# Optimization experiments

Measured on AMD Instinct MI355X. Metric: run time of the kernel, lower is better.

The kernel has to match this reference:

```python
import jax, jax.numpy as jnp
import numpy as np

B, T, E = 4, 2048, 1024
H, HS = 16, 64
FF = 4 * E
EPS = 1e-5


def _layer_norm(x, g, b):
    mu = jnp.mean(x, axis=-1, keepdims=True)
    var = jnp.mean(jnp.square(x - mu), axis=-1, keepdims=True)
    return (x - mu) * jax.lax.rsqrt(var + EPS) * g + b


def setup_inputs() -> dict:
    key = jax.random.key(0)
    ks = jax.random.split(key, 8)
    s_e = 1.0 / np.sqrt(E)
    s_hs = 1.0 / np.sqrt(H * HS)
    s_ff = 1.0 / np.sqrt(FF)
    return {
        "x": jax.random.normal(ks[0], (B, T, E), dtype=jnp.float32),
        # weights stored as [in, out] (transpose of torch's [out, in])
        "qkv_w": jax.random.uniform(ks[1], (E, 3 * H * HS), minval=-s_e, maxval=s_e),
        "attn_proj_w": jax.random.uniform(ks[2], (H * HS, E), minval=-s_hs, maxval=s_hs),
        "attn_proj_b": jax.random.uniform(ks[3], (E,), minval=-s_hs, maxval=s_hs),
        "ln1_g": jnp.ones((E,), jnp.float32),
        "ln1_b": jnp.zeros((E,), jnp.float32),
        "ln2_g": jnp.ones((E,), jnp.float32),
        "ln2_b": jnp.zeros((E,), jnp.float32),
        "ff_w1": jax.random.uniform(ks[4], (E, FF), minval=-s_e, maxval=s_e),
        "ff_b1": jax.random.uniform(ks[5], (FF,), minval=-s_e, maxval=s_e),
        "ff_w2": jax.random.uniform(ks[6], (FF, E), minval=-s_ff, maxval=s_ff),
        "ff_b2": jax.random.uniform(ks[7], (E,), minval=-s_ff, maxval=s_ff),
    }


def reference(x, qkv_w, attn_proj_w, attn_proj_b, ln1_g, ln1_b, ln2_g, ln2_b,
              ff_w1, ff_b1, ff_w2, ff_b2):
    b, t, _ = x.shape
    # --- pre-LN causal self-attention ---
    h = _layer_norm(x, ln1_g, ln1_b)
    qkv = h @ qkv_w                                  # [B,T,3*H*HS]
    q, k, v = jnp.split(qkv, 3, axis=-1)
    q = q.reshape(b, t, H, HS).transpose(0, 2, 1, 3)  # [B,H,T,HS]
    k = k.reshape(b, t, H, HS).transpose(0, 2, 1, 3)
    v = v.reshape(b, t, H, HS).transpose(0, 2, 1, 3)
    scores = jnp.einsum('bhqd,bhkd->bhqk', q, k) * (HS ** -0.5)
    causal = jnp.tril(jnp.ones((t, t), dtype=bool))
    scores = jnp.where(causal, scores, -jnp.inf)
    attn = jax.nn.softmax(scores, axis=-1)
    out = jnp.einsum('bhqk,bhkd->bhqd', attn, v)      # [B,H,T,HS]
    out = out.transpose(0, 2, 1, 3).reshape(b, t, H * HS)
    x = x + out @ attn_proj_w + attn_proj_b
    # --- pre-LN feed-forward ---
    h2 = _layer_norm(x, ln2_g, ln2_b)
    ff = jax.nn.relu(h2 @ ff_w1 + ff_b1) @ ff_w2 + ff_b2
    return x + ff
```

## Files before the change

kernel.cpp:

```cpp
#include <hip/hip_runtime.h>
#include <math.h>

#define B_ 4
#define T_ 2048
#define E_ 1024
#define H_ 16
#define HS_ 64
#define FF_ 4096
#define M_ (B_ * T_)
#define QKV3_ (3 * H_ * HS_)

typedef short bf16x8 __attribute__((ext_vector_type(8)));
typedef short bf16x4 __attribute__((ext_vector_type(4)));
typedef float f32x4 __attribute__((ext_vector_type(4)));

__device__ __forceinline__ unsigned short f2bf(float f) {
    unsigned int u = __float_as_uint(f);
    return (unsigned short)((u + 0x7fffu + ((u >> 16) & 1u)) >> 16);
}

__device__ __forceinline__ void gload16(const void* g, void* l) {
    __builtin_amdgcn_global_load_lds(
        (const __attribute__((address_space(1))) void*)g,
        (__attribute__((address_space(3))) void*)l, 16, 0, 0);
}

__global__ __launch_bounds__(256) void wT_bf16(const float* __restrict__ W,
                                               unsigned short* __restrict__ WT,
                                               int K, int N) {
    __shared__ float t[32][33];
    const int n0 = blockIdx.x * 32, k0 = blockIdx.y * 32;
    const int tid = threadIdx.x;
#pragma unroll
    for (int i = 0; i < 4; i++) {
        const int idx = i * 256 + tid;
        const int r = idx >> 5, c = idx & 31;
        t[r][c] = W[(size_t)(k0 + r) * N + n0 + c];
    }
    __syncthreads();
#pragma unroll
    for (int i = 0; i < 4; i++) {
        const int idx = i * 256 + tid;
        const int n = idx >> 5, k = idx & 31;
        WT[(size_t)(n0 + n) * K + k0 + k] = f2bf(t[k][n]);
    }
}

__global__ __launch_bounds__(256) void ln_bf16(const float* __restrict__ x,
                                               const float* __restrict__ g,
                                               const float* __restrict__ b,
                                               unsigned short* __restrict__ out) {
    const int row = blockIdx.x;
    const int tid = threadIdx.x;
    const float4 v = ((const float4*)(x + (size_t)row * E_))[tid];
    float s = v.x + v.y + v.z + v.w;
    float ss = v.x * v.x + v.y * v.y + v.z * v.z + v.w * v.w;
    for (int off = 32; off > 0; off >>= 1) {
        s += __shfl_down(s, off);
        ss += __shfl_down(ss, off);
    }
    __shared__ float rs[4], rss[4];
    const int wid = tid >> 6;
    if ((tid & 63) == 0) { rs[wid] = s; rss[wid] = ss; }
    __syncthreads();
    const float tot = rs[0] + rs[1] + rs[2] + rs[3];
    const float tot2 = rss[0] + rss[1] + rss[2] + rss[3];
    const float mean = tot * (1.0f / E_);
    const float var = tot2 * (1.0f / E_) - mean * mean;
    const float rstd = rsqrtf(var + 1e-5f);
    const float4 gv = ((const float4*)g)[tid];
    const float4 bv = ((const float4*)b)[tid];
    ushort4 o;
    o.x = f2bf((v.x - mean) * rstd * gv.x + bv.x);
    o.y = f2bf((v.y - mean) * rstd * gv.y + bv.y);
    o.z = f2bf((v.z - mean) * rstd * gv.z + bv.z);
    o.w = f2bf((v.w - mean) * rstd * gv.w + bv.w);
    ((ushort4*)(out + (size_t)row * E_))[tid] = o;
}

template <bool BIASF, bool RELU, bool RES, bool OUTBF16>
__global__ __launch_bounds__(256) void gemm_bf16(
    const unsigned short* __restrict__ A,
    const unsigned short* __restrict__ BT,
    const float* __restrict__ bias,
    const float* __restrict__ res,
    float* __restrict__ Cf,
    unsigned short* __restrict__ Cb,
    int M, int N, int K) {
    __shared__ unsigned short Al[128 * 64];
    __shared__ unsigned short Bl[128 * 64];

    const int tid = threadIdx.x;
    const int lane = tid & 63;
    const int w = tid >> 6;
    const int wm = w >> 1, wn = w & 1;

    const int gx = gridDim.x;
    const int nwg = gx * gridDim.y;
    const int lin = blockIdx.y * gx + blockIdx.x;
    const int cpx = nwg >> 3;
    const int swz = (lin & 7) * cpx + (lin >> 3);
    const int rowBase = (swz / gx) * 128, colBase = (swz % gx) * 128;

    f32x4 acc[4][4];
#pragma unroll
    for (int mt = 0; mt < 4; mt++)
#pragma unroll
        for (int nt = 0; nt < 4; nt++)
#pragma unroll
            for (int r = 0; r < 4; r++) acc[mt][nt][r] = 0.0f;

    const size_t rA = (size_t)rowBase * K;
    const size_t rB = (size_t)colBase * K;
    const int lm = lane & 15;
    const int kg = lane >> 4;

    for (int k0 = 0; k0 < K; k0 += 64) {
#pragma unroll
        for (int i = 0; i < 4; i++) {
            const int c = (w * 4 + i) * 64 + lane;
            const int r = c >> 3, s = c & 7;
            const int ss = s ^ (r & 7);
            gload16(A + rA + (size_t)r * K + k0 + ss * 8, (char*)Al + c * 16);
            gload16(BT + rB + (size_t)r * K + k0 + ss * 8, (char*)Bl + c * 16);
        }
        __syncthreads();

#pragma unroll
        for (int ks = 0; ks < 2; ks++) {
            bf16x8 af[4], bfr[4];
#pragma unroll
            for (int mt = 0; mt < 4; mt++)
                af[mt] = *(const bf16x8*)(Al + (wm * 64 + mt * 16 + lm) * 64 +
                                          (((ks * 4 + kg) ^ (lm & 7)) * 8));
#pragma unroll
            for (int nt = 0; nt < 4; nt++)
                bfr[nt] = *(const bf16x8*)(Bl + (wn * 64 + nt * 16 + lm) * 64 +
                                           (((ks * 4 + kg) ^ (lm & 7)) * 8));
#pragma unroll
            for (int mt = 0; mt < 4; mt++)
#pragma unroll
                for (int nt = 0; nt < 4; nt++)
                    acc[mt][nt] = __builtin_amdgcn_mfma_f32_16x16x32_bf16(
                        af[mt], bfr[nt], acc[mt][nt], 0, 0, 0);
        }
        __syncthreads();
    }

#pragma unroll
    for (int mt = 0; mt < 4; mt++) {
#pragma unroll
        for (int nt = 0; nt < 4; nt++) {
            const int cg = colBase + wn * 64 + nt * 16 + lm;
#pragma unroll
            for (int r = 0; r < 4; r++) {
                const int rg = rowBase + wm * 64 + mt * 16 + kg * 4 + r;
                float v = acc[mt][nt][r];
                if (BIASF) v += bias[cg];
                if (RELU) v = fmaxf(v, 0.0f);
                if (RES) v += res[(size_t)rg * N + cg];
                if (OUTBF16) Cb[(size_t)rg * N + cg] = f2bf(v);
                else Cf[(size_t)rg * N + cg] = v;
            }
        }
    }
}

__global__ __launch_bounds__(256) void attn_mfma2(const unsigned short* __restrict__ qkv,
                                                  unsigned short* __restrict__ out) {
    __shared__ unsigned short Ks[64 * 64];
    __shared__ unsigned short Vt[64 * 72];

    const int tid = threadIdx.x;
    const int lane = tid & 63;
    const int w = tid >> 6;
    const int lm = lane & 15;
    const int kg = lane >> 4;
    const int qt = 15 - blockIdx.x;
    const int bh = blockIdx.y;
    const int b = bh >> 4, h = bh & 15;
    const int bT = b * T_;
    const int q0w = qt * 128 + w * 32;
    const float K1 = 0.18033688011f;

    bf16x8 qf[2][2];
#pragma unroll
    for (int qg = 0; qg < 2; qg++) {
        const size_t qo = (size_t)(bT + q0w + qg * 16 + lm) * QKV3_ + h * HS_;
#pragma unroll
        for (int dc = 0; dc < 2; dc++)
            qf[qg][dc] = *(const bf16x8*)(qkv + qo + dc * 32 + kg * 8);
    }

    f32x4 o[2][4];
#pragma unroll
    for (int qg = 0; qg < 2; qg++)
#pragma unroll
        for (int dt = 0; dt < 4; dt++)
#pragma unroll
            for (int r = 0; r < 4; r++) o[qg][dt][r] = 0.0f;
    float m2[2] = {-INFINITY, -INFINITY};
    float l[2] = {0.0f, 0.0f};

    const int rK = tid >> 3, chK = tid & 7;
    const int sK = (chK ^ (rK & 7)) * 8;
    const int rp = tid >> 3, chV = tid & 7;
    const int vws = (2 * rp) ^ (chV << 2);

    const size_t hK = E_ + h * HS_;
    const size_t hV = 2 * E_ + h * HS_;
    bf16x8 kA, kB, vA, vB;

#define LOADT(kvb)                                                                          \
    do {                                                                                    \
        kA = *(const bf16x8*)(qkv + (size_t)(bT + (kvb) + rK) * QKV3_ + hK + chK * 8);      \
        kB = *(const bf16x8*)(qkv + (size_t)(bT + (kvb) + rK + 32) * QKV3_ + hK + chK * 8); \
        vA = *(const bf16x8*)(qkv + (size_t)(bT + (kvb) + 2 * rp) * QKV3_ + hV + chV * 8);  \
        vB = *(const bf16x8*)(qkv + (size_t)(bT + (kvb) + 2 * rp + 1) * QKV3_ + hV + chV * 8); \
    } while (0)

    const int nt = 2 * (qt + 1);
    LOADT(0);
    for (int t = 0; t < nt; t++) {
        const int kvbase = t * 64;
        __syncthreads();
        *(bf16x8*)(Ks + rK * 64 + sK) = kA;
        *(bf16x8*)(Ks + (rK + 32) * 64 + sK) = kB;
#pragma unroll
        for (int i = 0; i < 8; i++) {
            const unsigned int pv = (unsigned int)(unsigned short)vA[i] |
                                    ((unsigned int)(unsigned short)vB[i] << 16);
            *(unsigned int*)(Vt + (chV * 8 + i) * 72 + vws) = pv;
        }
        if (t + 1 < nt) LOADT((t + 1) * 64);
        __syncthreads();
        if (kvbase > q0w + 31) continue;

        bf16x8 af[4][2];
#pragma unroll
        for (int g = 0; g < 4; g++)
#pragma unroll
            for (int dc = 0; dc < 2; dc++)
                af[g][dc] = *(const bf16x8*)(Ks + (g * 16 + lm) * 64 +
                                             (((dc * 4 + kg) ^ (lm & 7)) * 8));

        bf16x8 pa[2][2];
#pragma unroll
        for (int qg = 0; qg < 2; qg++) {
            f32x4 z = {0.0f, 0.0f, 0.0f, 0.0f};
            f32x4 s[4];
#pragma unroll
            for (int g = 0; g < 4; g++) {
                s[g] = __builtin_amdgcn_mfma_f32_16x16x32_bf16(af[g][0], qf[qg][0], z, 0, 0, 0);
                s[g] = __builtin_amdgcn_mfma_f32_16x16x32_bf16(af[g][1], qf[qg][1], s[g], 0, 0, 0);
            }
            const int qrow = q0w + qg * 16 + lm;
            float sv[16];
#pragma unroll
            for (int g = 0; g < 4; g++)
#pragma unroll
                for (int r = 0; r < 4; r++) sv[g * 4 + r] = s[g][r];
            if (kvbase + 63 > q0w + qg * 16) {
#pragma unroll
                for (int g = 0; g < 4; g++)
#pragma unroll
                    for (int r = 0; r < 4; r++) {
                        const int kv = kvbase + g * 16 + kg * 4 + r;
                        if (kv > qrow) sv[g * 4 + r] = -INFINITY;
                    }
            }
            float mx = sv[0];
#pragma unroll
            for (int j = 1; j < 16; j++) mx = fmaxf(mx, sv[j]);
            mx = fmaxf(mx, __shfl_xor(mx, 16));
            mx = fmaxf(mx, __shfl_xor(mx, 32));
            const float mx2 = mx * K1;
            if (!__all(m2[qg] > -1e30f && mx2 <= m2[qg] + 11.5f)) {
                const float m2new = fmaxf(m2[qg], mx2);
                const float alpha = exp2f(m2[qg] - m2new);
#pragma unroll
                for (int r = 0; r < 4; r++) {
                    const float ar = __shfl(alpha, kg * 4 + r);
#pragma unroll
                    for (int dt = 0; dt < 4; dt++) o[qg][dt][r] *= ar;
                }
                l[qg] *= alpha;
                m2[qg] = m2new;
            }
            float p[16], ls = 0.0f;
#pragma unroll
            for (int j = 0; j < 16; j++) {
                p[j] = exp2f(fmaf(sv[j], K1, -m2[qg]));
                ls += p[j];
            }
            ls += __shfl_xor(ls, 16);
            ls += __shfl_xor(ls, 32);
            l[qg] += ls;
#pragma unroll
            for (int j = 0; j < 8; j++) {
                ((unsigned short*)&pa[qg][0])[j] = f2bf(p[j]);
                ((unsigned short*)&pa[qg][1])[j] = f2bf(p[8 + j]);
            }
        }

#pragma unroll
        for (int dt = 0; dt < 4; dt++) {
            const int drow = dt * 16 + lm;
            const unsigned short* vrow = Vt + drow * 72;
            const int xo = (kg * 4) ^ (((drow >> 3) & 7) << 2);
#pragma unroll
            for (int c = 0; c < 2; c++) {
                const bf16x4 lo = *(const bf16x4*)(vrow + c * 32 + xo);
                const bf16x4 hi = *(const bf16x4*)(vrow + c * 32 + (xo ^ 16));
                const bf16x8 vf = __builtin_shufflevector(lo, hi, 0, 1, 2, 3, 4, 5, 6, 7);
                o[0][dt] = __builtin_amdgcn_mfma_f32_16x16x32_bf16(pa[0][c], vf, o[0][dt], 0, 0, 0);
                o[1][dt] = __builtin_amdgcn_mfma_f32_16x16x32_bf16(pa[1][c], vf, o[1][dt], 0, 0, 0);
            }
        }
    }
#undef LOADT

#pragma unroll
    for (int qg = 0; qg < 2; qg++)
#pragma unroll
        for (int r = 0; r < 4; r++) {
            const float li = 1.0f / __shfl(l[qg], kg * 4 + r);
            const size_t ro = (size_t)(bT + q0w + qg * 16 + kg * 4 + r) * E_ + h * HS_;
#pragma unroll
            for (int dt = 0; dt < 4; dt++)
                out[ro + dt * 16 + lm] = f2bf(o[qg][dt][r] * li);
        }
}

extern "C" void kernel_launch(void* const* d_in, const int* in_sizes, int n_in,
                              void* d_out, int out_size, void* d_ws, size_t ws_size,
                              hipStream_t stream) {
    const float* x           = (const float*)d_in[0];
    const float* qkv_w       = (const float*)d_in[1];
    const float* attn_proj_w = (const float*)d_in[2];
    const float* attn_proj_b = (const float*)d_in[3];
    const float* ln1_g       = (const float*)d_in[4];
    const float* ln1_b       = (const float*)d_in[5];
    const float* ln2_g       = (const float*)d_in[6];
    const float* ln2_b       = (const float*)d_in[7];
    const float* ff_w1       = (const float*)d_in[8];
    const float* ff_b1       = (const float*)d_in[9];
    const float* ff_w2       = (const float*)d_in[10];
    const float* ff_b2       = (const float*)d_in[11];
    float* out = (float*)d_out;
    char* wsb = (char*)d_ws;

    unsigned short* wqkvT  = (unsigned short*)(wsb + 0);
    unsigned short* wprojT = (unsigned short*)(wsb + 6291456);
    unsigned short* wff1T  = (unsigned short*)(wsb + 8388608);
    unsigned short* wff2T  = (unsigned short*)(wsb + 16777216);
    unsigned short* hbuf   = (unsigned short*)(wsb + 25165824);
    unsigned short* attnb  = (unsigned short*)(wsb + 41943040);
    unsigned short* qkvb   = (unsigned short*)(wsb + 58720256);
    unsigned short* ff1b   = qkvb;

    wT_bf16<<<dim3(QKV3_ / 32, E_ / 32), 256, 0, stream>>>(qkv_w, wqkvT, E_, QKV3_);
    wT_bf16<<<dim3(E_ / 32, E_ / 32), 256, 0, stream>>>(attn_proj_w, wprojT, E_, E_);
    wT_bf16<<<dim3(FF_ / 32, E_ / 32), 256, 0, stream>>>(ff_w1, wff1T, E_, FF_);
    wT_bf16<<<dim3(E_ / 32, FF_ / 32), 256, 0, stream>>>(ff_w2, wff2T, FF_, E_);

    ln_bf16<<<M_, 256, 0, stream>>>(x, ln1_g, ln1_b, hbuf);
    gemm_bf16<false, false, false, true><<<dim3(QKV3_ / 128, M_ / 128), 256, 0, stream>>>(
        hbuf, wqkvT, nullptr, nullptr, nullptr, qkvb, M_, QKV3_, E_);
    attn_mfma2<<<dim3(T_ / 128, B_ * H_), 256, 0, stream>>>(qkvb, attnb);
    gemm_bf16<true, false, true, false><<<dim3(E_ / 128, M_ / 128), 256, 0, stream>>>(
        attnb, wprojT, attn_proj_b, x, out, nullptr, M_, E_, E_);
    ln_bf16<<<M_, 256, 0, stream>>>(out, ln2_g, ln2_b, hbuf);
    gemm_bf16<true, true, false, true><<<dim3(FF_ / 128, M_ / 128), 256, 0, stream>>>(
        hbuf, wff1T, ff_b1, nullptr, nullptr, ff1b, M_, FF_, E_);
    gemm_bf16<true, false, true, false><<<dim3(E_ / 128, M_ / 128), 256, 0, stream>>>(
        ff1b, wff2T, ff_b2, out, out, nullptr, M_, E_, FF_);
    (void)ws_size; (void)in_sizes; (void)n_in; (void)out_size;
}
```

Baseline: 586.8 us.

## Triple-buffer GEMM with 128x256 tiles, 512 threads; double-buffer attention K/V

The GEMM now uses 512-thread blocks with 128x256 tiles and a three-stage LDS ring. Global-to-LDS loads run two k-steps ahead, with explicit vmcnt waits, raw barriers and setprio around the MFMA blocks, to hide memory latency behind compute. The attention kernel double-buffers its K/V LDS tiles, so one barrier per iteration replaces two, and it rewrites the max and sum reductions as trees for more ILP. The GEMM LDS footprint grows to about 144KB, which limits occupancy to one block per CU, and the hand-written wait counts are fragile.

```diff
diff --git a/kernel.cpp b/kernel.cpp
--- a/kernel.cpp
+++ b/kernel.cpp
@@ -78,8 +78,16 @@
     ((ushort4*)(out + (size_t)row * E_))[tid] = o;
 }
 
+__device__ __forceinline__ void stage_half(const unsigned short* __restrict__ G,
+                                           size_t rbase, int K, int k0,
+                                           unsigned short* lds, int c) {
+    const int r = c >> 3, s = c & 7;
+    gload16(G + rbase + (size_t)r * K + k0 + ((s ^ (r & 7)) * 8),
+            (char*)lds + c * 16);
+}
+
 template <bool BIASF, bool RELU, bool RES, bool OUTBF16>
-__global__ __launch_bounds__(256) void gemm_bf16(
+__global__ __launch_bounds__(512) void gemm_v3(
     const unsigned short* __restrict__ A,
     const unsigned short* __restrict__ BT,
     const float* __restrict__ bias,
@@ -87,64 +95,98 @@
     float* __restrict__ Cf,
     unsigned short* __restrict__ Cb,
     int M, int N, int K) {
-    __shared__ unsigned short Al[128 * 64];
-    __shared__ unsigned short Bl[128 * 64];
+    __shared__ unsigned short As[3][128 * 64];
+    __shared__ unsigned short Bs[3][256 * 64];
 
     const int tid = threadIdx.x;
     const int lane = tid & 63;
     const int w = tid >> 6;
-    const int wm = w >> 1, wn = w & 1;
+    const int wm = w >> 2, wn = w & 3;
+    const int lm = lane & 15;
+    const int kg = lane >> 4;
 
     const int gx = gridDim.x;
     const int nwg = gx * gridDim.y;
     const int lin = blockIdx.y * gx + blockIdx.x;
     const int cpx = nwg >> 3;
     const int swz = (lin & 7) * cpx + (lin >> 3);
-    const int rowBase = (swz / gx) * 128, colBase = (swz % gx) * 128;
-
-    f32x4 acc[4][4];
-#pragma unroll
-    for (int mt = 0; mt < 4; mt++)
-#pragma unroll
-        for (int nt = 0; nt < 4; nt++)
-#pragma unroll
-            for (int r = 0; r < 4; r++) acc[mt][nt][r] = 0.0f;
+    const int rowBase = (swz / gx) * 128, colBase = (swz % gx) * 256;
 
     const size_t rA = (size_t)rowBase * K;
     const size_t rB = (size_t)colBase * K;
-    const int lm = lane & 15;
-    const int kg = lane >> 4;
-
-    for (int k0 = 0; k0 < K; k0 += 64) {
-#pragma unroll
-        for (int i = 0; i < 4; i++) {
-            const int c = (w * 4 + i) * 64 + lane;
-            const int r = c >> 3, s = c & 7;
-            const int ss = s ^ (r & 7);
-            gload16(A + rA + (size_t)r * K + k0 + ss * 8, (char*)Al + c * 16);
-            gload16(BT + rB + (size_t)r * K + k0 + ss * 8, (char*)Bl + c * 16);
-        }
-        __syncthreads();
-
-#pragma unroll
-        for (int ks = 0; ks < 2; ks++) {
+
+    f32x4 acc[4][4];
+#pragma unroll
+    for (int mt = 0; mt < 4; mt++)
+#pragma unroll
+        for (int nt = 0; nt < 4; nt++)
+#pragma unroll
+            for (int r = 0; r < 4; r++) acc[mt][nt][r] = 0.0f;
+
+    const int nk = K >> 6;
+#pragma unroll
+    for (int h = 0; h < 2; h++) {
+        stage_half(A, rA, K, 0, As[0], h * 512 + tid);
+        stage_half(BT, rB, K, 0, Bs[0], h * 1024 + tid);
+        stage_half(BT, rB, K, 0, Bs[0], h * 1024 + 512 + tid);
+    }
+#pragma unroll
+    for (int h = 0; h < 2; h++) {
+        stage_half(A, rA, K, 64, As[1], h * 512 + tid);
+        stage_half(BT, rB, K, 64, Bs[1], h * 1024 + tid);
+        stage_half(BT, rB, K, 64, Bs[1], h * 1024 + 512 + tid);
+    }
+    asm volatile("s_waitcnt vmcnt(6)" ::: "memory");
+    __builtin_amdgcn_s_barrier();
+    __builtin_amdgcn_sched_barrier(0);
+
+    for (int t = 0; t < nk; ++t) {
+        const int cur = t % 3;
+        const int nx2 = (t + 2) % 3;
+        const bool doStage = (t + 2 < nk);
+#pragma unroll
+        for (int ks = 0; ks < 2; ++ks) {
             bf16x8 af[4], bfr[4];
 #pragma unroll
-            for (int mt = 0; mt < 4; mt++)
-                af[mt] = *(const bf16x8*)(Al + (wm * 64 + mt * 16 + lm) * 64 +
-                                          (((ks * 4 + kg) ^ (lm & 7)) * 8));
-#pragma unroll
-            for (int nt = 0; nt < 4; nt++)
-                bfr[nt] = *(const bf16x8*)(Bl + (wn * 64 + nt * 16 + lm) * 64 +
-                                           (((ks * 4 + kg) ^ (lm & 7)) * 8));
+            for (int mt = 0; mt < 4; mt++) {
+                const int r = wm * 64 + mt * 16 + lm;
+                af[mt] = *(const bf16x8*)(As[cur] + r * 64 +
+                                          (((ks * 4 + kg) ^ (r & 7)) * 8));
+            }
+#pragma unroll
+            for (int nt = 0; nt < 4; nt++) {
+                const int r = wn * 64 + nt * 16 + lm;
+                bfr[nt] = *(const bf16x8*)(Bs[cur] + r * 64 +
+                                           (((ks * 4 + kg) ^ (r & 7)) * 8));
+            }
+            if (doStage) {
+                stage_half(A, rA, K, (t + 2) * 64, As[nx2], ks * 512 + tid);
+                stage_half(BT, rB, K, (t + 2) * 64, Bs[nx2], ks * 1024 + tid);
+                stage_half(BT, rB, K, (t + 2) * 64, Bs[nx2], ks * 1024 + 512 + tid);
+            }
+            __builtin_amdgcn_s_barrier();
+            __builtin_amdgcn_sched_barrier(0);
+            __builtin_amdgcn_s_setprio(1);
 #pragma unroll
             for (int mt = 0; mt < 4; mt++)
 #pragma unroll
                 for (int nt = 0; nt < 4; nt++)
                     acc[mt][nt] = __builtin_amdgcn_mfma_f32_16x16x32_bf16(
                         af[mt], bfr[nt], acc[mt][nt], 0, 0, 0);
-        }
-        __syncthreads();
+            __builtin_amdgcn_s_setprio(0);
+            if (ks == 0) {
+                __builtin_amdgcn_s_barrier();
+                __builtin_amdgcn_sched_barrier(0);
+            }
+        }
+        if (t + 2 < nk) {
+            asm volatile("s_waitcnt vmcnt(6)" ::: "memory");
+        } else if (t + 1 < nk) {
+            asm volatile("s_waitcnt vmcnt(0)" ::: "memory");
+        }
+        __builtin_amdgcn_sched_barrier(0);
+        __builtin_amdgcn_s_barrier();
+        __builtin_amdgcn_sched_barrier(0);
     }
 
 #pragma unroll
@@ -166,10 +208,10 @@
     }
 }
 
-__global__ __launch_bounds__(256) void attn_mfma2(const unsigned short* __restrict__ qkv,
+__global__ __launch_bounds__(256) void attn_mfma3(const unsigned short* __restrict__ qkv,
                                                   unsigned short* __restrict__ out) {
-    __shared__ unsigned short Ks[64 * 64];
-    __shared__ unsigned short Vt[64 * 72];
+    __shared__ unsigned short Ks[2][64 * 64];
+    __shared__ unsigned short Vt[2][64 * 72];
 
     const int tid = threadIdx.x;
     const int lane = tid & 63;
@@ -223,17 +265,19 @@
     LOADT(0);
     for (int t = 0; t < nt; t++) {
         const int kvbase = t * 64;
-        __syncthreads();
-        *(bf16x8*)(Ks + rK * 64 + sK) = kA;
-        *(bf16x8*)(Ks + (rK + 32) * 64 + sK) = kB;
+        const int cb = t & 1;
+        *(bf16x8*)(Ks[cb] + rK * 64 + sK) = kA;
+        *(bf16x8*)(Ks[cb] + (rK + 32) * 64 + sK) = kB;
 #pragma unroll
         for (int i = 0; i < 8; i++) {
             const unsigned int pv = (unsigned int)(unsigned short)vA[i] |
                                     ((unsigned int)(unsigned short)vB[i] << 16);
-            *(unsigned int*)(Vt + (chV * 8 + i) * 72 + vws) = pv;
+            *(unsigned int*)(Vt[cb] + (chV * 8 + i) * 72 + vws) = pv;
         }
         if (t + 1 < nt) LOADT((t + 1) * 64);
-        __syncthreads();
+        asm volatile("s_waitcnt lgkmcnt(0)" ::: "memory");
+        __builtin_amdgcn_s_barrier();
+        __builtin_amdgcn_sched_barrier(0);
         if (kvbase > q0w + 31) continue;
 
         bf16x8 af[4][2];
@@ -241,7 +285,7 @@
         for (int g = 0; g < 4; g++)
 #pragma unroll
             for (int dc = 0; dc < 2; dc++)
-                af[g][dc] = *(const bf16x8*)(Ks + (g * 16 + lm) * 64 +
+                af[g][dc] = *(const bf16x8*)(Ks[cb] + (g * 16 + lm) * 64 +
                                              (((dc * 4 + kg) ^ (lm & 7)) * 8));
 
         bf16x8 pa[2][2];
@@ -269,12 +313,14 @@
                         if (kv > qrow) sv[g * 4 + r] = -INFINITY;
                     }
             }
-            float mx = sv[0];
-#pragma unroll
-            for (int j = 1; j < 16; j++) mx = fmaxf(mx, sv[j]);
-            mx = fmaxf(mx, __shfl_xor(mx, 16));
-            mx = fmaxf(mx, __shfl_xor(mx, 32));
-            const float mx2 = mx * K1;
+            const float mx = fmaxf(
+                fmaxf(fmaxf(fmaxf(sv[0], sv[1]), fmaxf(sv[2], sv[3])),
+                      fmaxf(fmaxf(sv[4], sv[5]), fmaxf(sv[6], sv[7]))),
+                fmaxf(fmaxf(fmaxf(sv[8], sv[9]), fmaxf(sv[10], sv[11])),
+                      fmaxf(fmaxf(sv[12], sv[13]), fmaxf(sv[14], sv[15]))));
+            float mxw = fmaxf(mx, __shfl_xor(mx, 16));
+            mxw = fmaxf(mxw, __shfl_xor(mxw, 32));
+            const float mx2 = mxw * K1;
             if (!__all(m2[qg] > -1e30f && mx2 <= m2[qg] + 11.5f)) {
                 const float m2new = fmaxf(m2[qg], mx2);
                 const float alpha = exp2f(m2[qg] - m2new);
@@ -287,12 +333,11 @@
                 l[qg] *= alpha;
                 m2[qg] = m2new;
             }
-            float p[16], ls = 0.0f;
-#pragma unroll
-            for (int j = 0; j < 16; j++) {
-                p[j] = exp2f(fmaf(sv[j], K1, -m2[qg]));
-                ls += p[j];
-            }
+            float p[16];
+#pragma unroll
+            for (int j = 0; j < 16; j++) p[j] = exp2f(fmaf(sv[j], K1, -m2[qg]));
+            float ls = (((p[0] + p[1]) + (p[2] + p[3])) + ((p[4] + p[5]) + (p[6] + p[7]))) +
+                       (((p[8] + p[9]) + (p[10] + p[11])) + ((p[12] + p[13]) + (p[14] + p[15])));
             ls += __shfl_xor(ls, 16);
             ls += __shfl_xor(ls, 32);
             l[qg] += ls;
@@ -306,7 +351,7 @@
 #pragma unroll
         for (int dt = 0; dt < 4; dt++) {
             const int drow = dt * 16 + lm;
-            const unsigned short* vrow = Vt + drow * 72;
+            const unsigned short* vrow = Vt[cb] + drow * 72;
             const int xo = (kg * 4) ^ (((drow >> 3) & 7) << 2);
 #pragma unroll
             for (int c = 0; c < 2; c++) {
@@ -365,15 +410,15 @@
     wT_bf16<<<dim3(E_ / 32, FF_ / 32), 256, 0, stream>>>(ff_w2, wff2T, FF_, E_);
 
     ln_bf16<<<M_, 256, 0, stream>>>(x, ln1_g, ln1_b, hbuf);
-    gemm_bf16<false, false, false, true><<<dim3(QKV3_ / 128, M_ / 128), 256, 0, stream>>>(
+    gemm_v3<false, false, false, true><<<dim3(QKV3_ / 256, M_ / 128), 512, 0, stream>>>(
         hbuf, wqkvT, nullptr, nullptr, nullptr, qkvb, M_, QKV3_, E_);
-    attn_mfma2<<<dim3(T_ / 128, B_ * H_), 256, 0, stream>>>(qkvb, attnb);
-    gemm_bf16<true, false, true, false><<<dim3(E_ / 128, M_ / 128), 256, 0, stream>>>(
+    attn_mfma3<<<dim3(T_ / 128, B_ * H_), 256, 0, stream>>>(qkvb, attnb);
+    gemm_v3<true, false, true, false><<<dim3(E_ / 256, M_ / 128), 512, 0, stream>>>(
         attnb, wprojT, attn_proj_b, x, out, nullptr, M_, E_, E_);
     ln_bf16<<<M_, 256, 0, stream>>>(out, ln2_g, ln2_b, hbuf);
-    gemm_bf16<true, true, false, true><<<dim3(FF_ / 128, M_ / 128), 256, 0, stream>>>(
+    gemm_v3<true, true, false, true><<<dim3(FF_ / 256, M_ / 128), 512, 0, stream>>>(
         hbuf, wff1T, ff_b1, nullptr, nullptr, ff1b, M_, FF_, E_);
-    gemm_bf16<true, false, true, false><<<dim3(E_ / 128, M_ / 128), 256, 0, stream>>>(
+    gemm_v3<true, false, true, false><<<dim3(E_ / 256, M_ / 128), 512, 0, stream>>>(
         ff1b, wff2T, ff_b2, out, out, nullptr, M_, E_, FF_);
     (void)ws_size; (void)in_sizes; (void)n_in; (void)out_size;
 }
```

New measurement: 570.7 us. 1.03x faster.
